# Kernel optimization log

Measured on AMD Instinct MI355X. Metric: run time of the kernel, lower is better.

The kernel has to match this reference:

```python
import jax, jax.numpy as jnp
import numpy as np

B, C, H, W = 4, 64, 128, 128
CQ = C // 8
EPS = 1e-5


def setup_inputs() -> dict:
    key = jax.random.key(0)
    ks = jax.random.split(key, 20)
    r = lambda k, shape, s=0.05: jax.random.normal(k, shape, dtype=jnp.float32) * s
    return {
        "x1": jax.random.normal(ks[0], (B, C, H, W), dtype=jnp.float32),
        "x2": jax.random.normal(ks[1], (B, C, H, W), dtype=jnp.float32),
        # 1x1 convs are plain channel matmuls: weight (out, in), bias (out,)
        "wqA": r(ks[2], (CQ, C)), "bqA": r(ks[3], (CQ,)),
        "wkA": r(ks[4], (CQ, C)), "bkA": r(ks[5], (CQ,)),
        "wvA": r(ks[6], (C, C)),  "bvA": r(ks[7], (C,)),
        "wqB": r(ks[8], (CQ, C)), "bqB": r(ks[9], (CQ,)),
        "wkB": r(ks[10], (CQ, C)), "bkB": r(ks[11], (CQ,)),
        "wvB": r(ks[12], (C, C)),  "bvB": r(ks[13], (C,)),
        "gA": r(ks[14], (1,), 0.1), "gB": r(ks[15], (1,), 0.1),
        "wp": r(ks[16], (C, C)), "bp": r(ks[17], (C,)),
        "bn_g": jnp.ones((C,), dtype=jnp.float32),
        "bn_b": jnp.zeros((C,), dtype=jnp.float32),
    }


def _conv1(x, w, b):
    # 1x1 conv over NCHW == per-pixel channel matmul
    return jnp.einsum('oi,bihw->bohw', w, x) + b[None, :, None, None]


def _axial(q, k, v):
    # criss-cross attention: for each pixel, attend over its row and column,
    # with the column (H) self-position masked to -inf, joint softmax over H+W.
    h = q.shape[2]
    eH = jnp.einsum('bciw,bcjw->biwj', q, k)            # [B,H,W,H] column scores
    eH = jnp.where(jnp.eye(h, dtype=bool)[:, None, :], -jnp.inf, eH)
    eW = jnp.einsum('bchi,bchj->bhij', q, k)            # [B,H,W,W] row scores
    att = jax.nn.softmax(jnp.concatenate([eH, eW], axis=3), axis=3)
    oH = jnp.einsum('bcjw,biwj->bciw', v, att[..., :h])
    oW = jnp.einsum('bchj,bhij->bchi', v, att[..., h:])
    return oH + oW


def _forward(x1, x2, wqA, bqA, wkA, bkA, wvA, bvA, wqB, bqB, wkB, bkB, wvB, bvB,
             gA, gB, wp, bp, bn_g, bn_b):
    # branch A: query from x2, key/value from x1
    out_A = _axial(_conv1(x2, wqA, bqA), _conv1(x1, wkA, bkA), _conv1(x1, wvA, bvA))
    # branch B: query/key/value all from x1
    out_B = _axial(_conv1(x1, wqB, bqB), _conv1(x1, wkB, bkB), _conv1(x1, wvB, bvB))
    diff = jnp.abs(out_A - out_B)
    p = jax.nn.gelu(_conv1(diff, wp, bp), approximate=False)
    # BatchNorm2d in training mode: batch statistics, biased variance
    m = p.mean(axis=(0, 2, 3), keepdims=True)
    v = ((p - m) ** 2).mean(axis=(0, 2, 3), keepdims=True)
    out = (p - m) / jnp.sqrt(v + EPS) * bn_g[None, :, None, None] + bn_b[None, :, None, None]
    return gA[0] * out_A + x1 + out, gB[0] * out_B + x2 + out


def reference(x1, x2, wqA, bqA, wkA, bkA, wvA, bvA, wqB, bqB, wkB, bkB, wvB, bvB,
              gA, gB, wp, bp, bn_g, bn_b):
    return _forward(x1, x2, wqA, bqA, wkA, bkA, wvA, bvA, wqB, bqB, wkB, bkB,
                    wvB, bvB, gA, gB, wp, bp, bn_g, bn_b)
```

## Files before the change

### kernel.cpp

```cpp
#include <hip/hip_runtime.h>


#define NE 4194304ull

typedef __attribute__((ext_vector_type(8))) short short8;
typedef __attribute__((ext_vector_type(4))) float f32x4;

#define HD __device__ __forceinline__

HD float b2f(unsigned short u) { union { unsigned int i; float f; } v; v.i = ((unsigned int)u) << 16; return v.f; }
HD unsigned short f2b(float x) {
  union { float f; unsigned int i; } v; v.f = x;
  unsigned int r = v.i + 0x7FFFu + ((v.i >> 16) & 1u);
  return (unsigned short)(r >> 16);
}

HD float erf_fast(float x) {
  const float ax = fabsf(x);
  const float t = 1.0f / (1.0f + 0.3275911f * ax);
  const float poly = ((((1.061405429f*t - 1.453152027f)*t + 1.421413741f)*t
                       - 0.284496736f)*t + 0.254829592f)*t;
  const float y = 1.0f - poly * __expf(-ax*ax);
  return copysignf(y, x);
}

HD unsigned short ldbf(const void* s0, int i, int f) {
  return f ? f2b(((const float*)s0)[i]) : ((const unsigned short*)s0)[i];
}

__global__ __launch_bounds__(256) void prelude_kernel(
    const void* x1,
    const void* wqA, const void* bqA, const void* wkA, const void* bkA,
    const void* wvA, const void* bvA, const void* wqB, const void* bqB,
    const void* wkB, const void* bkB, const void* wvB, const void* bvB,
    const void* wp, const void* bp, const void* gA, const void* gB,
    const void* bng, const void* bnb,
    int* flag, unsigned short* wout)
{
  __shared__ int s;
  if (threadIdx.x == 0) s = 0;
  __syncthreads();
  const float a = fabsf(b2f(((const unsigned short*)x1)[threadIdx.x]));
  if (a > 1000.0f) atomicOr(&s, 1);
  __syncthreads();
  const int f = s;
  if (blockIdx.x == 0 && threadIdx.x == 0) *flag = f;

  const void* srcs[18] = {wqA,bqA,wkA,bkA,wvA,bvA,wqB,bqB,wkB,bkB,wvB,bvB,wp,bp,gA,gB,bng,bnb};
  const int   ns[18]   = {512,  8,512,  8,4096, 64,512,  8,512,  8,4096, 64,4096,64, 1, 1, 64, 64};
  unsigned short* wqkv = wout + 14696;
  float* wbias = (float*)(wout + 25960);

  const int gstride = gridDim.x * 256;
  for (int idx = blockIdx.x*256 + threadIdx.x; idx < 26136; idx += gstride) {
    if (idx < 14690) {
      int off = idx, k2 = 0;
      while (off >= ns[k2]) { off -= ns[k2]; ++k2; }
      wout[idx] = ldbf(srcs[k2], off, f);
    } else if (idx >= 25960) {
      const int i3 = idx - 25960, mt = i3 >> 4, r = i3 & 15;
      float val = 0.0f;
      if (mt == 0)      { if (r < 8) val = b2f(ldbf(bqA, r, f)); }
      else if (mt == 1) { val = b2f((r < 8) ? ldbf(bkA, r, f) : ldbf(bqB, r - 8, f)); }
      else if (mt == 2) { if (r < 8) val = b2f(ldbf(bkB, r, f)); }
      else if (mt < 7)  { val = b2f(ldbf(bvA, (mt-3)*16 + r, f)); }
      else              { val = b2f(ldbf(bvB, (mt-7)*16 + r, f)); }
      wbias[i3] = val;
    } else if (idx >= 14696) {
      const int i2 = idx - 14696;
      const int mt = i2 >> 10, rem = i2 & 1023, r = rem >> 6, ci = rem & 63;
      unsigned short val = 0;
      if (mt == 0)      { if (r < 8) val = ldbf(wqA, r*64 + ci, f); }
      else if (mt == 1) { val = (r < 8) ? ldbf(wkA, r*64 + ci, f) : ldbf(wqB, (r-8)*64 + ci, f); }
      else if (mt == 2) { if (r < 8) val = ldbf(wkB, r*64 + ci, f); }
      else if (mt < 7)  { val = ldbf(wvA, ((mt-3)*16 + r)*64 + ci, f); }
      else              { val = ldbf(wvB, ((mt-7)*16 + r)*64 + ci, f); }
      wqkv[i2] = val;
    }
  }
}

__global__ __launch_bounds__(256) void qkv_kernel(
    const void* __restrict__ x1v, const void* __restrict__ x2v, const int* __restrict__ flag,
    const unsigned short* __restrict__ wqkv, const float* __restrict__ wbias,
    unsigned short* __restrict__ q, unsigned short* __restrict__ k,
    unsigned short* __restrict__ v)
{
  const int hp = blockIdx.x, b = blockIdx.y;
  const int h0 = hp*2;
  const int tid = threadIdx.x, lane = tid & 63, w4 = tid >> 6;
  const int col = lane & 15, quad = lane >> 4;
  const int f32m = *flag;
  __shared__ __align__(16) char smem[33792];
  unsigned short* Xb = (unsigned short*)smem;
  unsigned short* S0 = (unsigned short*)smem;
  unsigned short* S1 = (unsigned short*)(smem + 8448);
  const size_t gb = (size_t)b*1048576 + (size_t)h0*128;

  short8 Bc[2][8];
  #pragma unroll
  for (int pass = 0; pass < 2; ++pass) {
    const void* xv = pass ? x2v : x1v;
    for (int t = tid; t < 2048; t += 256) {
      const int c = t >> 5, rem = t & 31, hh = rem >> 4, w8 = (rem & 15)*8;
      const int n = hh*128 + w8;
      const size_t a = gb + (size_t)c*16384 + (size_t)hh*128 + w8;
      unsigned short vals[8];
      if (f32m) {
        const float* xf = (const float*)xv;
        const float4 f0 = *(const float4*)(xf + a);
        const float4 f1 = *(const float4*)(xf + a + 4);
        vals[0]=f2b(f0.x); vals[1]=f2b(f0.y); vals[2]=f2b(f0.z); vals[3]=f2b(f0.w);
        vals[4]=f2b(f1.x); vals[5]=f2b(f1.y); vals[6]=f2b(f1.z); vals[7]=f2b(f1.w);
      } else {
        const uint4 u = *(const uint4*)((const unsigned short*)xv + a);
        vals[0]=(unsigned short)(u.x & 0xffff); vals[1]=(unsigned short)(u.x >> 16);
        vals[2]=(unsigned short)(u.y & 0xffff); vals[3]=(unsigned short)(u.y >> 16);
        vals[4]=(unsigned short)(u.z & 0xffff); vals[5]=(unsigned short)(u.z >> 16);
        vals[6]=(unsigned short)(u.w & 0xffff); vals[7]=(unsigned short)(u.w >> 16);
      }
      #pragma unroll
      for (int i = 0; i < 8; ++i) Xb[(n + i)*66 + c] = vals[i];
    }
    __syncthreads();
    const unsigned int* U = (const unsigned int*)Xb;
    #pragma unroll
    for (int nt = 0; nt < 4; ++nt)
      #pragma unroll
      for (int ks = 0; ks < 2; ++ks) {
        const int n = w4*64 + nt*16 + col;
        const int base = n*33 + (ks*32 + quad*8)/2;
        union { unsigned int u32[4]; short8 s; } p;
        #pragma unroll
        for (int jj = 0; jj < 4; ++jj) p.u32[jj] = U[base + jj];
        Bc[pass][nt*2 + ks] = p.s;
      }
    __syncthreads();
  }

  #pragma unroll
  for (int mt = 0; mt < 11; ++mt) {
    f32x4 acc[4];
    #pragma unroll
    for (int nt = 0; nt < 4; ++nt) acc[nt] = (f32x4){0.f, 0.f, 0.f, 0.f};
    #pragma unroll
    for (int ks = 0; ks < 2; ++ks) {
      union { uint4 u; short8 s; } A;
      A.u = *(const uint4*)(wqkv + mt*1024 + col*64 + ks*32 + quad*8);
      #pragma unroll
      for (int nt = 0; nt < 4; ++nt)
        acc[nt] = __builtin_amdgcn_mfma_f32_16x16x32_bf16(
            A.s, (mt == 0) ? Bc[1][nt*2 + ks] : Bc[0][nt*2 + ks], acc[nt], 0, 0, 0);
    }
    float bias[4];
    #pragma unroll
    for (int r = 0; r < 4; ++r) bias[r] = wbias[mt*16 + quad*4 + r];
    unsigned short* S = (mt & 1) ? S1 : S0;
    #pragma unroll
    for (int nt = 0; nt < 4; ++nt)
      #pragma unroll
      for (int r = 0; r < 4; ++r) {
        const int row = quad*4 + r;
        const int nloc = w4*64 + nt*16 + col;
        S[row*264 + nloc] = f2b(acc[nt][r] + bias[r]);
      }
    __syncthreads();
    if (mt < 3) {
      const int nloc = tid;
      const int pixg = h0*128 + nloc;
      union { unsigned short u[8]; uint4 v4; } P;
      #pragma unroll
      for (int r = 0; r < 8; ++r) P.u[r] = S[r*264 + nloc];
      if (mt == 0) {
        *(uint4*)(q + ((size_t)b*16384 + pixg)*8) = P.v4;
      } else if (mt == 1) {
        *(uint4*)(k + ((size_t)b*16384 + pixg)*8) = P.v4;
        #pragma unroll
        for (int r = 0; r < 8; ++r) P.u[r] = S[(8 + r)*264 + nloc];
        *(uint4*)(q + ((size_t)(4 + b)*16384 + pixg)*8) = P.v4;
      } else {
        *(uint4*)(k + ((size_t)(4 + b)*16384 + pixg)*8) = P.v4;
      }
    } else {
      const int vm = (mt >= 7) ? mt - 7 : mt - 3;
      const int z  = (mt >= 7) ? 4 + b : b;
      const int cl = tid >> 4, u = tid & 15;
      const int co = vm*16 + cl;
      const uint4 a0 = *(const uint4*)&S[cl*264 + u*16];
      const uint4 a1 = *(const uint4*)&S[cl*264 + u*16 + 8];
      unsigned short* dst = v + ((size_t)(z*64 + co)*16384 + (size_t)h0*128 + u*16);
      *(uint4*)dst = a0;
      *(uint4*)(dst + 8) = a1;
    }
  }
}

__global__ __launch_bounds__(256) void transpose_v(
    const unsigned short* __restrict__ vStd, unsigned short* __restrict__ vT)
{
  const int tile = blockIdx.x, c = blockIdx.y, z = blockIdx.z;
  const int h0 = (tile & 3) * 32, w0 = (tile >> 2) * 32;
  const size_t base = ((size_t)z*64 + c) * 16384;
  __shared__ unsigned short T[32][33];
  const int tid = threadIdx.x;
  for (int idx = tid; idx < 1024; idx += 256) {
    const int r = idx >> 5, cc = idx & 31;
    T[r][cc] = vStd[base + (size_t)(h0 + r)*128 + (w0 + cc)];
  }
  __syncthreads();
  for (int idx = tid; idx < 1024; idx += 256) {
    const int r = idx >> 5, cc = idx & 31;
    vT[base + (size_t)(w0 + r)*128 + (h0 + cc)] = T[cc][r];
  }
}

__global__ __launch_bounds__(256) void pv_kernel(
    const unsigned short* __restrict__ q, const unsigned short* __restrict__ k,
    const unsigned short* __restrict__ vStd, const unsigned short* __restrict__ vT,
    float* __restrict__ outBrF, float* __restrict__ oColF,
    float* __restrict__ lRow, float* __restrict__ lCol)
{
  const int X = blockIdx.x, b = blockIdx.y;
  const int br = blockIdx.z & 1, dir = blockIdx.z >> 1;
  const int tid = threadIdx.x, lane = tid & 63, w4 = tid >> 6;
  const int col = lane & 15, quad = lane >> 4;
  const int z = br*4 + b;
  const size_t b4h = (size_t)z * 128;
  __shared__ __align__(16) char smemA[34048];
  __shared__ __align__(16) char smemB[16384];
  unsigned short* P = (unsigned short*)smemA;
  float* Dst = (float*)smemA;
  uint4* Ks = (uint4*)smemB;
  uint4* Vl = (uint4*)smemB;

  if (tid < 128) {
    const int j = tid;
    const size_t pix = (b4h + (dir ? X : j))*128 + (dir ? j : X);
    Ks[j] = *(const uint4*)(k + pix*8);
  }
  __syncthreads();

  const uint4 zero4 = {0u, 0u, 0u, 0u};
  short8 Afr[2];
  #pragma unroll
  for (int ib2 = 0; ib2 < 2; ++ib2) {
    uint4 a = zero4;
    if (quad == 0) {
      const int m = (w4*2 + ib2)*16 + col;
      const size_t pix = (b4h + (dir ? X : m))*128 + (dir ? m : X);
      a = *(const uint4*)(q + pix*8);
    }
    union { uint4 u; short8 s; } cv; cv.u = a; Afr[ib2] = cv.s;
  }
  float lsum[2][4];
  #pragma unroll
  for (int ib2 = 0; ib2 < 2; ++ib2)
    #pragma unroll
    for (int r = 0; r < 4; ++r) lsum[ib2][r] = 0.0f;
  #pragma unroll
  for (int nb = 0; nb < 8; ++nb) {
    uint4 bu = (quad == 0) ? Ks[nb*16 + col] : zero4;
    union { uint4 u; short8 s; } bv; bv.u = bu;
    f32x4 sA = __builtin_amdgcn_mfma_f32_16x16x32_bf16(Afr[0], bv.s, (f32x4){0.f,0.f,0.f,0.f}, 0, 0, 0);
    f32x4 sB = __builtin_amdgcn_mfma_f32_16x16x32_bf16(Afr[1], bv.s, (f32x4){0.f,0.f,0.f,0.f}, 0, 0, 0);
    const int j = nb*16 + col;
    #pragma unroll
    for (int ib2 = 0; ib2 < 2; ++ib2) {
      const int mbase = (w4*2 + ib2)*16 + quad*4;
      #pragma unroll
      for (int r = 0; r < 4; ++r) {
        const int m = mbase + r;
        const float sv = ib2 ? sB[r] : sA[r];
        float p = 0.0f;
        if (dir || (j != m)) p = __expf(sv);
        lsum[ib2][r] += p;
        P[m*132 + j] = f2b(p);
      }
    }
  }
  #pragma unroll
  for (int ib2 = 0; ib2 < 2; ++ib2)
    #pragma unroll
    for (int r = 0; r < 4; ++r) {
      float s = lsum[ib2][r];
      s += __shfl_xor(s, 1); s += __shfl_xor(s, 2);
      s += __shfl_xor(s, 4); s += __shfl_xor(s, 8);
      if (col == 0) {
        const int m = (w4*2 + ib2)*16 + quad*4 + r;
        float* lOut = dir ? lRow : lCol;
        lOut[((size_t)z*128 + X)*128 + m] = s;
      }
    }
  __syncthreads();

  short8 af[2][4];
  #pragma unroll
  for (int ib2 = 0; ib2 < 2; ++ib2) {
    const int m = (w4*2 + ib2)*16 + col;
    #pragma unroll
    for (int kb = 0; kb < 4; ++kb) {
      const int j0 = kb*32 + quad*8;
      union { uint2 u[2]; short8 s; } pk;
      pk.u[0] = *(const uint2*)&P[m*132 + j0];
      pk.u[1] = *(const uint2*)&P[m*132 + j0 + 4];
      af[ib2][kb] = pk.s;
    }
  }
  const unsigned short* vsrc = dir ? vStd : vT;
  const size_t vbase = ((size_t)z*64)*16384 + (size_t)X*128;
  for (int t = tid; t < 1024; t += 256) {
    const int vl = t & 63, nb = (t >> 6) & 3, kb = t >> 8;
    const int c = nb*16 + (vl & 15), j0 = kb*32 + ((vl >> 4) << 3);
    Vl[t] = *(const uint4*)(vsrc + vbase + (size_t)c*16384 + j0);
  }
  __syncthreads();

  f32x4 acc[2][4];
  #pragma unroll
  for (int i2 = 0; i2 < 2; ++i2)
    #pragma unroll
    for (int nb = 0; nb < 4; ++nb) acc[i2][nb] = (f32x4){0.f, 0.f, 0.f, 0.f};
  #pragma unroll
  for (int nb = 0; nb < 4; ++nb)
    #pragma unroll
    for (int kb = 0; kb < 4; ++kb) {
      const short8 bfr = *(short8*)&Vl[(kb*4 + nb)*64 + lane];
      acc[0][nb] = __builtin_amdgcn_mfma_f32_16x16x32_bf16(af[0][kb], bfr, acc[0][nb], 0, 0, 0);
      acc[1][nb] = __builtin_amdgcn_mfma_f32_16x16x32_bf16(af[1][kb], bfr, acc[1][nb], 0, 0, 0);
    }
  __syncthreads();

  #pragma unroll
  for (int i2 = 0; i2 < 2; ++i2)
    #pragma unroll
    for (int nb = 0; nb < 4; ++nb)
      #pragma unroll
      for (int r = 0; r < 4; ++r) {
        const int mm = (w4*2 + i2)*16 + ((lane >> 4) << 2) + r;
        const int cc = nb*16 + (lane & 15);
        Dst[cc*133 + mm] = acc[i2][nb][r];
      }
  __syncthreads();
  float* dst = dir ? outBrF : oColF;
  for (int t = tid; t < 8192; t += 256) {
    const int cc = t >> 7, mm = t & 127;
    dst[vbase + (size_t)cc*16384 + mm] = Dst[cc*133 + mm];
  }
}

__global__ __launch_bounds__(256) void combine_kernel(
    const float* __restrict__ oColU, const float* __restrict__ lRow,
    const float* __restrict__ lCol, float* __restrict__ outBr)
{
  const int tile = blockIdx.x, z = blockIdx.y, cg = blockIdx.z;
  const int h0 = (tile & 3) * 32, w0 = (tile >> 2) * 32, c0 = cg*8;
  const int tid = threadIdx.x;
  __shared__ float Tl[32][33];
  __shared__ __align__(16) float inv[32][36];
  __shared__ __align__(16) float T4[4][32][36];
  const size_t lzb = (size_t)z * 16384;
  {
    const int w = tid >> 3, h4 = (tid & 7)*4;
    const float4 vc = *(const float4*)(lCol + lzb + (size_t)(w0 + w)*128 + h0 + h4);
    Tl[w][h4+0] = vc.x; Tl[w][h4+1] = vc.y; Tl[w][h4+2] = vc.z; Tl[w][h4+3] = vc.w;
  }
  __syncthreads();
  {
    const int h = tid >> 3, w4 = (tid & 7)*4;
    const float4 lr = *(const float4*)(lRow + lzb + (size_t)(h0 + h)*128 + w0 + w4);
    float4 iv;
    iv.x = 1.0f / (lr.x + Tl[w4+0][h]);
    iv.y = 1.0f / (lr.y + Tl[w4+1][h]);
    iv.z = 1.0f / (lr.z + Tl[w4+2][h]);
    iv.w = 1.0f / (lr.w + Tl[w4+3][h]);
    *(float4*)&inv[h][w4] = iv;
  }
  __syncthreads();
  #pragma unroll
  for (int half = 0; half < 2; ++half) {
    for (int t = tid; t < 1024; t += 256) {
      const int ch = t >> 8, rem = t & 255, w = rem >> 3, h4 = (rem & 7)*4;
      const int c = c0 + half*4 + ch;
      const float4 vc = *(const float4*)(oColU + ((size_t)(z*64 + c))*16384
                                         + (size_t)(w0 + w)*128 + h0 + h4);
      *(float4*)&T4[ch][w][h4] = vc;
    }
    __syncthreads();
    for (int t = tid; t < 1024; t += 256) {
      const int ch = t >> 8, rem = t & 255, h = rem >> 3, w4 = (rem & 7)*4;
      const int c = c0 + half*4 + ch;
      const size_t off = ((size_t)(z*64 + c))*16384 + (size_t)(h0 + h)*128 + w0 + w4;
      float4 o = *(const float4*)(outBr + off);
      const float4 iv = *(const float4*)&inv[h][w4];
      o.x = (o.x + T4[ch][w4+0][h]) * iv.x;
      o.y = (o.y + T4[ch][w4+1][h]) * iv.y;
      o.z = (o.z + T4[ch][w4+2][h]) * iv.z;
      o.w = (o.w + T4[ch][w4+3][h]) * iv.w;
      *(float4*)(outBr + off) = o;
    }
    __syncthreads();
  }
}

__global__ __launch_bounds__(256) void proj_kernel(
    const float* __restrict__ outA, const float* __restrict__ outB,
    const unsigned short* __restrict__ wp, const unsigned short* __restrict__ bp,
    float* __restrict__ pbuf, float* __restrict__ part)
{
  const int h = blockIdx.x, b = blockIdx.y, wh = blockIdx.z, tid = threadIdx.x;
  const int blk = ((h*4 + b)*2 + wh);
  __shared__ __align__(16) float diffs[64][64];
  for (int idx = tid; idx < 4096; idx += 256) {
    const int c = idx >> 6, w = idx & 63;
    const size_t off = ((size_t)(b*64 + c)*128 + h)*128 + wh*64 + w;
    diffs[c][w] = fabsf(outA[off] - outB[off]);
  }
  __syncthreads();
  const int cog = tid >> 5, wl = tid & 31;
  float acc[8][2];
  #pragma unroll
  for (int c8 = 0; c8 < 8; ++c8) { acc[c8][0] = 0.f; acc[c8][1] = 0.f; }
  for (int cb = 0; cb < 8; ++cb) {
    uint4 wrow[8];
    #pragma unroll
    for (int c8 = 0; c8 < 8; ++c8) wrow[c8] = *(const uint4*)&wp[(cog*8 + c8)*64 + cb*8];
    #pragma unroll
    for (int t = 0; t < 8; ++t) {
      const int ci = cb*8 + t;
      const float d0 = diffs[ci][wl], d1 = diffs[ci][wl + 32];
      #pragma unroll
      for (int c8 = 0; c8 < 8; ++c8) {
        const float wf = b2f(((const unsigned short*)&wrow[c8])[t]);
        acc[c8][0] += wf*d0; acc[c8][1] += wf*d1;
      }
    }
  }
  #pragma unroll
  for (int c8 = 0; c8 < 8; ++c8) {
    const int co = cog*8 + c8;
    const float bias = b2f(bp[co]);
    const size_t pb = ((size_t)(b*64 + co)*128 + h)*128 + wh*64;
    float s1 = 0.f, s2 = 0.f;
    #pragma unroll
    for (int t = 0; t < 2; ++t) {
      const float x = acc[c8][t] + bias;
      const float g = 0.5f * x * (1.0f + erf_fast(x * 0.70710678118f));
      pbuf[pb + wl + t*32] = g;
      s1 += g; s2 += g*g;
    }
    #pragma unroll
    for (int off = 16; off >= 1; off >>= 1) { s1 += __shfl_xor(s1, off); s2 += __shfl_xor(s2, off); }
    if (wl == 0) {
      part[(size_t)co*1024 + blk] = s1;
      part[(size_t)(64 + co)*1024 + blk] = s2;
    }
  }
}

__global__ __launch_bounds__(256) void reduce_kernel(
    const float* __restrict__ part, float* __restrict__ bnAcc)
{
  const int stat = blockIdx.x, tid = threadIdx.x;
  const float4 v = *(const float4*)(part + (size_t)stat*1024 + tid*4);
  float s = v.x + v.y + v.z + v.w;
  #pragma unroll
  for (int off = 32; off >= 1; off >>= 1) s += __shfl_xor(s, off);
  __shared__ float ws4[4];
  if ((tid & 63) == 0) ws4[tid >> 6] = s;
  __syncthreads();
  if (tid == 0) bnAcc[stat] = ws4[0] + ws4[1] + ws4[2] + ws4[3];
}

__global__ __launch_bounds__(256) void final_kernel(
    const float* __restrict__ pbuf, const float* __restrict__ outA, const float* __restrict__ outB,
    const void* __restrict__ x1v, const void* __restrict__ x2v, const int* __restrict__ flag,
    const unsigned short* __restrict__ gA, const unsigned short* __restrict__ gB,
    const unsigned short* __restrict__ bng, const unsigned short* __restrict__ bnb,
    const float* __restrict__ bnAcc, void* __restrict__ outv)
{
  const int f32m = *flag;
  const int idx = (blockIdx.x * 256 + threadIdx.x) * 4;
  const int c = (idx >> 14) & 63;
  const float invN = 1.0f / 65536.0f;
  const float s1 = bnAcc[c], s2 = bnAcc[64 + c];
  const float mean = s1 * invN;
  const float var = s2 * invN - mean*mean;
  const float scale = rsqrtf(var + 1e-5f) * b2f(bng[c]);
  const float beta = b2f(bnb[c]);
  const float ga = b2f(gA[0]), gb = b2f(gB[0]);
  const float4 p4 = *(const float4*)(pbuf + idx);
  const float4 a4 = *(const float4*)(outA + idx);
  const float4 b4 = *(const float4*)(outB + idx);
  float p[4] = {p4.x, p4.y, p4.z, p4.w};
  float a[4] = {a4.x, a4.y, a4.z, a4.w};
  float bb[4] = {b4.x, b4.y, b4.z, b4.w};
  float xa[4], xb[4];
  if (f32m) {
    const float4 t1 = *(const float4*)((const float*)x1v + idx);
    const float4 t2 = *(const float4*)((const float*)x2v + idx);
    xa[0]=t1.x; xa[1]=t1.y; xa[2]=t1.z; xa[3]=t1.w;
    xb[0]=t2.x; xb[1]=t2.y; xb[2]=t2.z; xb[3]=t2.w;
  } else {
    const uint2 x1u = *(const uint2*)((const unsigned short*)x1v + idx);
    const uint2 x2u = *(const uint2*)((const unsigned short*)x2v + idx);
    xa[0] = b2f((unsigned short)(x1u.x & 0xffff)); xa[1] = b2f((unsigned short)(x1u.x >> 16));
    xa[2] = b2f((unsigned short)(x1u.y & 0xffff)); xa[3] = b2f((unsigned short)(x1u.y >> 16));
    xb[0] = b2f((unsigned short)(x2u.x & 0xffff)); xb[1] = b2f((unsigned short)(x2u.x >> 16));
    xb[2] = b2f((unsigned short)(x2u.y & 0xffff)); xb[3] = b2f((unsigned short)(x2u.y >> 16));
  }
  float o1f[4], o2f[4];
  #pragma unroll
  for (int t = 0; t < 4; ++t) {
    const float nv = (p[t] - mean)*scale + beta;
    o1f[t] = ga*a[t] + xa[t] + nv;
    o2f[t] = gb*bb[t] + xb[t] + nv;
  }
  if (f32m) {
    float* of = (float*)outv;
    *(float4*)(of + idx)      = (float4){o1f[0], o1f[1], o1f[2], o1f[3]};
    *(float4*)(of + NE + idx) = (float4){o2f[0], o2f[1], o2f[2], o2f[3]};
  } else {
    unsigned short* oh = (unsigned short*)outv;
    uint2 u1, u2;
    u1.x = (unsigned int)f2b(o1f[0]) | ((unsigned int)f2b(o1f[1]) << 16);
    u1.y = (unsigned int)f2b(o1f[2]) | ((unsigned int)f2b(o1f[3]) << 16);
    u2.x = (unsigned int)f2b(o2f[0]) | ((unsigned int)f2b(o2f[1]) << 16);
    u2.y = (unsigned int)f2b(o2f[2]) | ((unsigned int)f2b(o2f[3]) << 16);
    *(uint2*)(oh + idx) = u1;
    *(uint2*)(oh + NE + idx) = u2;
  }
}

extern "C" void kernel_launch(void* const* d_in, const int* in_sizes, int n_in,
                              void* d_out, int out_size, void* d_ws, size_t ws_size,
                              hipStream_t stream)
{
  const void* x1  = d_in[0];
  const void* x2  = d_in[1];

  char* ws = (char*)d_ws;
  const size_t MB = 1048576ull;
  unsigned short* q     = (unsigned short*)(ws);
  unsigned short* kk    = (unsigned short*)(ws + 2*MB);
  float* lRow           = (float*)(ws + 4*MB);
  float* lCol           = (float*)(ws + 4*MB + 512*1024);
  unsigned short* vStd  = (unsigned short*)(ws + 6*MB);
  unsigned short* vT    = (unsigned short*)(ws + 22*MB);
  float* outBr          = (float*)(ws + 38*MB);
  float* oColF          = (float*)(ws + 70*MB);
  float* pbuf           = (float*)(ws + 70*MB);
  float* part           = (float*)(ws + 86*MB);
  float* bnAcc          = (float*)(ws + 102*MB);
  int*   flag           = (int*)(ws + 102*MB + 512);
  unsigned short* wC    = (unsigned short*)(ws + 102*MB + 1024);

  prelude_kernel<<<64, 256, 0, stream>>>(
      x1, d_in[2], d_in[3], d_in[4], d_in[5], d_in[6], d_in[7], d_in[8], d_in[9],
      d_in[10], d_in[11], d_in[12], d_in[13], d_in[16], d_in[17], d_in[14], d_in[15],
      d_in[18], d_in[19], flag, wC);
  qkv_kernel<<<dim3(64, 4), 256, 0, stream>>>(
      x1, x2, flag, wC + 14696, (const float*)(wC + 25960), q, kk, vStd);
  transpose_v<<<dim3(16, 64, 8), 256, 0, stream>>>(vStd, vT);
  pv_kernel<<<dim3(128, 4, 4), 256, 0, stream>>>(q, kk, vStd, vT, outBr, oColF, lRow, lCol);
  combine_kernel<<<dim3(16, 8, 8), 256, 0, stream>>>(oColF, lRow, lCol, outBr);
  proj_kernel<<<dim3(128, 4, 2), 256, 0, stream>>>(outBr, outBr + NE, wC + 10400, wC + 14496, pbuf, part);
  reduce_kernel<<<128, 256, 0, stream>>>(part, bnAcc);
  final_kernel<<<4096, 256, 0, stream>>>(pbuf, outBr, outBr + NE, x1, x2, flag,
                                         wC + 14560, wC + 14561, wC + 14562, wC + 14626,
                                         bnAcc, d_out);
}
```

Before: 232.2 us.

## Store attention branch outputs in bf16 and move projection onto MFMA

```diff
diff --git a/kernel.cpp b/kernel.cpp
--- a/kernel.cpp
+++ b/kernel.cpp
@@ -217,7 +217,7 @@
 __global__ __launch_bounds__(256) void pv_kernel(
     const unsigned short* __restrict__ q, const unsigned short* __restrict__ k,
     const unsigned short* __restrict__ vStd, const unsigned short* __restrict__ vT,
-    float* __restrict__ outBrF, float* __restrict__ oColF,
+    unsigned short* __restrict__ outBrH, unsigned short* __restrict__ oColH,
     float* __restrict__ lRow, float* __restrict__ lCol)
 {
   const int X = blockIdx.x, b = blockIdx.y;
@@ -341,16 +341,20 @@
         Dst[cc*133 + mm] = acc[i2][nb][r];
       }
   __syncthreads();
-  float* dst = dir ? outBrF : oColF;
-  for (int t = tid; t < 8192; t += 256) {
-    const int cc = t >> 7, mm = t & 127;
-    dst[vbase + (size_t)cc*16384 + mm] = Dst[cc*133 + mm];
+  unsigned short* dsth = dir ? outBrH : oColH;
+  for (int t = tid; t < 2048; t += 256) {
+    const int cc = t >> 5, mm4 = (t & 31) * 4;
+    const float* sp = &Dst[cc*133 + mm4];
+    uint2 u;
+    u.x = (unsigned int)f2b(sp[0]) | ((unsigned int)f2b(sp[1]) << 16);
+    u.y = (unsigned int)f2b(sp[2]) | ((unsigned int)f2b(sp[3]) << 16);
+    *(uint2*)(dsth + vbase + (size_t)cc*16384 + mm4) = u;
   }
 }
 
 __global__ __launch_bounds__(256) void combine_kernel(
-    const float* __restrict__ oColU, const float* __restrict__ lRow,
-    const float* __restrict__ lCol, float* __restrict__ outBr)
+    const unsigned short* __restrict__ oColU, const float* __restrict__ lRow,
+    const float* __restrict__ lCol, unsigned short* __restrict__ outBr)
 {
   const int tile = blockIdx.x, z = blockIdx.y, cg = blockIdx.z;
   const int h0 = (tile & 3) * 32, w0 = (tile >> 2) * 32, c0 = cg*8;
@@ -381,79 +385,121 @@
     for (int t = tid; t < 1024; t += 256) {
       const int ch = t >> 8, rem = t & 255, w = rem >> 3, h4 = (rem & 7)*4;
       const int c = c0 + half*4 + ch;
-      const float4 vc = *(const float4*)(oColU + ((size_t)(z*64 + c))*16384
-                                         + (size_t)(w0 + w)*128 + h0 + h4);
-      *(float4*)&T4[ch][w][h4] = vc;
+      const uint2 vc = *(const uint2*)(oColU + ((size_t)(z*64 + c))*16384
+                                       + (size_t)(w0 + w)*128 + h0 + h4);
+      float4 f;
+      f.x = b2f((unsigned short)(vc.x & 0xffff)); f.y = b2f((unsigned short)(vc.x >> 16));
+      f.z = b2f((unsigned short)(vc.y & 0xffff)); f.w = b2f((unsigned short)(vc.y >> 16));
+      *(float4*)&T4[ch][w][h4] = f;
     }
     __syncthreads();
     for (int t = tid; t < 1024; t += 256) {
       const int ch = t >> 8, rem = t & 255, h = rem >> 3, w4 = (rem & 7)*4;
       const int c = c0 + half*4 + ch;
       const size_t off = ((size_t)(z*64 + c))*16384 + (size_t)(h0 + h)*128 + w0 + w4;
-      float4 o = *(const float4*)(outBr + off);
+      const uint2 ov = *(const uint2*)(outBr + off);
       const float4 iv = *(const float4*)&inv[h][w4];
-      o.x = (o.x + T4[ch][w4+0][h]) * iv.x;
-      o.y = (o.y + T4[ch][w4+1][h]) * iv.y;
-      o.z = (o.z + T4[ch][w4+2][h]) * iv.z;
-      o.w = (o.w + T4[ch][w4+3][h]) * iv.w;
-      *(float4*)(outBr + off) = o;
+      float o0 = b2f((unsigned short)(ov.x & 0xffff));
+      float o1 = b2f((unsigned short)(ov.x >> 16));
+      float o2 = b2f((unsigned short)(ov.y & 0xffff));
+      float o3 = b2f((unsigned short)(ov.y >> 16));
+      o0 = (o0 + T4[ch][w4+0][h]) * iv.x;
+      o1 = (o1 + T4[ch][w4+1][h]) * iv.y;
+      o2 = (o2 + T4[ch][w4+2][h]) * iv.z;
+      o3 = (o3 + T4[ch][w4+3][h]) * iv.w;
+      uint2 u;
+      u.x = (unsigned int)f2b(o0) | ((unsigned int)f2b(o1) << 16);
+      u.y = (unsigned int)f2b(o2) | ((unsigned int)f2b(o3) << 16);
+      *(uint2*)(outBr + off) = u;
     }
     __syncthreads();
   }
 }
 
 __global__ __launch_bounds__(256) void proj_kernel(
-    const float* __restrict__ outA, const float* __restrict__ outB,
+    const unsigned short* __restrict__ outA, const unsigned short* __restrict__ outB,
     const unsigned short* __restrict__ wp, const unsigned short* __restrict__ bp,
     float* __restrict__ pbuf, float* __restrict__ part)
 {
-  const int h = blockIdx.x, b = blockIdx.y, wh = blockIdx.z, tid = threadIdx.x;
-  const int blk = ((h*4 + b)*2 + wh);
-  __shared__ __align__(16) float diffs[64][64];
-  for (int idx = tid; idx < 4096; idx += 256) {
-    const int c = idx >> 6, w = idx & 63;
-    const size_t off = ((size_t)(b*64 + c)*128 + h)*128 + wh*64 + w;
-    diffs[c][w] = fabsf(outA[off] - outB[off]);
-  }
-  __syncthreads();
-  const int cog = tid >> 5, wl = tid & 31;
-  float acc[8][2];
-  #pragma unroll
-  for (int c8 = 0; c8 < 8; ++c8) { acc[c8][0] = 0.f; acc[c8][1] = 0.f; }
-  for (int cb = 0; cb < 8; ++cb) {
-    uint4 wrow[8];
-    #pragma unroll
-    for (int c8 = 0; c8 < 8; ++c8) wrow[c8] = *(const uint4*)&wp[(cog*8 + c8)*64 + cb*8];
-    #pragma unroll
-    for (int t = 0; t < 8; ++t) {
-      const int ci = cb*8 + t;
-      const float d0 = diffs[ci][wl], d1 = diffs[ci][wl + 32];
-      #pragma unroll
-      for (int c8 = 0; c8 < 8; ++c8) {
-        const float wf = b2f(((const unsigned short*)&wrow[c8])[t]);
-        acc[c8][0] += wf*d0; acc[c8][1] += wf*d1;
-      }
-    }
-  }
-  #pragma unroll
-  for (int c8 = 0; c8 < 8; ++c8) {
-    const int co = cog*8 + c8;
-    const float bias = b2f(bp[co]);
-    const size_t pb = ((size_t)(b*64 + co)*128 + h)*128 + wh*64;
-    float s1 = 0.f, s2 = 0.f;
-    #pragma unroll
-    for (int t = 0; t < 2; ++t) {
-      const float x = acc[c8][t] + bias;
+  const int hp = blockIdx.x, b = blockIdx.y;
+  const int tid = threadIdx.x, lane = tid & 63, w4 = tid >> 6;
+  const int col = lane & 15, quad = lane >> 4;
+  __shared__ __align__(16) char smem[17408];
+  unsigned short* Xb = (unsigned short*)smem;
+  float* S = (float*)smem;
+
+  const size_t gb = (size_t)b*1048576 + (size_t)hp*64;
+  for (int t = tid; t < 512; t += 256) {
+    const int c = t >> 3, rem = t & 7;
+    const size_t a = gb + (size_t)c*16384 + rem*8;
+    const uint4 ua = *(const uint4*)(outA + a);
+    const uint4 ub = *(const uint4*)(outB + a);
+    const unsigned short* pa = (const unsigned short*)&ua;
+    const unsigned short* pb = (const unsigned short*)&ub;
+    const int n = rem*8;
+    #pragma unroll
+    for (int i = 0; i < 8; ++i)
+      Xb[(n + i)*66 + c] = f2b(fabsf(b2f(pa[i]) - b2f(pb[i])));
+  }
+  __syncthreads();
+
+  short8 Bc[8];
+  const unsigned int* U = (const unsigned int*)Xb;
+  #pragma unroll
+  for (int nt = 0; nt < 4; ++nt)
+    #pragma unroll
+    for (int ks = 0; ks < 2; ++ks) {
+      const int n = nt*16 + col;
+      const int base = n*33 + (ks*32 + quad*8)/2;
+      union { unsigned int u32[4]; short8 s; } p;
+      #pragma unroll
+      for (int jj = 0; jj < 4; ++jj) p.u32[jj] = U[base + jj];
+      Bc[nt*2 + ks] = p.s;
+    }
+  __syncthreads();
+
+  f32x4 acc[4];
+  #pragma unroll
+  for (int nt = 0; nt < 4; ++nt) acc[nt] = (f32x4){0.f, 0.f, 0.f, 0.f};
+  #pragma unroll
+  for (int ks = 0; ks < 2; ++ks) {
+    union { uint4 u; short8 s; } A;
+    A.u = *(const uint4*)(wp + (w4*16 + col)*64 + ks*32 + quad*8);
+    #pragma unroll
+    for (int nt = 0; nt < 4; ++nt)
+      acc[nt] = __builtin_amdgcn_mfma_f32_16x16x32_bf16(A.s, Bc[nt*2 + ks], acc[nt], 0, 0, 0);
+  }
+
+  float sg1[4] = {0.f, 0.f, 0.f, 0.f}, sg2[4] = {0.f, 0.f, 0.f, 0.f};
+  #pragma unroll
+  for (int nt = 0; nt < 4; ++nt)
+    #pragma unroll
+    for (int r = 0; r < 4; ++r) {
+      const float x = acc[nt][r] + b2f(bp[w4*16 + quad*4 + r]);
       const float g = 0.5f * x * (1.0f + erf_fast(x * 0.70710678118f));
-      pbuf[pb + wl + t*32] = g;
-      s1 += g; s2 += g*g;
-    }
-    #pragma unroll
-    for (int off = 16; off >= 1; off >>= 1) { s1 += __shfl_xor(s1, off); s2 += __shfl_xor(s2, off); }
-    if (wl == 0) {
-      part[(size_t)co*1024 + blk] = s1;
-      part[(size_t)(64 + co)*1024 + blk] = s2;
-    }
+      S[(w4*16 + quad*4 + r)*68 + nt*16 + col] = g;
+      sg1[r] += g; sg2[r] += g*g;
+    }
+  const int slot = hp*4 + b;
+  #pragma unroll
+  for (int r = 0; r < 4; ++r) {
+    float s1 = sg1[r], s2 = sg2[r];
+    s1 += __shfl_xor(s1, 1); s1 += __shfl_xor(s1, 2);
+    s1 += __shfl_xor(s1, 4); s1 += __shfl_xor(s1, 8);
+    s2 += __shfl_xor(s2, 1); s2 += __shfl_xor(s2, 2);
+    s2 += __shfl_xor(s2, 4); s2 += __shfl_xor(s2, 8);
+    if (col == 0) {
+      const int co = w4*16 + quad*4 + r;
+      part[(size_t)co*1024 + slot] = s1;
+      part[(size_t)(64 + co)*1024 + slot] = s2;
+    }
+  }
+  __syncthreads();
+
+  for (int t = tid; t < 1024; t += 256) {
+    const int row = t >> 4, px4 = (t & 15)*4;
+    const float4 v4 = *(const float4*)&S[row*68 + px4];
+    *(float4*)(pbuf + (size_t)(b*64 + row)*16384 + hp*64 + px4) = v4;
   }
 }
 
@@ -472,7 +518,8 @@
 }
 
 __global__ __launch_bounds__(256) void final_kernel(
-    const float* __restrict__ pbuf, const float* __restrict__ outA, const float* __restrict__ outB,
+    const float* __restrict__ pbuf,
+    const unsigned short* __restrict__ outAH, const unsigned short* __restrict__ outBH,
     const void* __restrict__ x1v, const void* __restrict__ x2v, const int* __restrict__ flag,
     const unsigned short* __restrict__ gA, const unsigned short* __restrict__ gB,
     const unsigned short* __restrict__ bng, const unsigned short* __restrict__ bnb,
@@ -489,11 +536,13 @@
   const float beta = b2f(bnb[c]);
   const float ga = b2f(gA[0]), gb = b2f(gB[0]);
   const float4 p4 = *(const float4*)(pbuf + idx);
-  const float4 a4 = *(const float4*)(outA + idx);
-  const float4 b4 = *(const float4*)(outB + idx);
+  const uint2 uA = *(const uint2*)(outAH + idx);
+  const uint2 uB = *(const uint2*)(outBH + idx);
   float p[4] = {p4.x, p4.y, p4.z, p4.w};
-  float a[4] = {a4.x, a4.y, a4.z, a4.w};
-  float bb[4] = {b4.x, b4.y, b4.z, b4.w};
+  float a[4] = { b2f((unsigned short)(uA.x & 0xffff)), b2f((unsigned short)(uA.x >> 16)),
+                 b2f((unsigned short)(uA.y & 0xffff)), b2f((unsigned short)(uA.y >> 16)) };
+  float bb[4] = { b2f((unsigned short)(uB.x & 0xffff)), b2f((unsigned short)(uB.x >> 16)),
+                  b2f((unsigned short)(uB.y & 0xffff)), b2f((unsigned short)(uB.y >> 16)) };
   float xa[4], xb[4];
   if (f32m) {
     const float4 t1 = *(const float4*)((const float*)x1v + idx);
@@ -546,8 +595,8 @@
   float* lCol           = (float*)(ws + 4*MB + 512*1024);
   unsigned short* vStd  = (unsigned short*)(ws + 6*MB);
   unsigned short* vT    = (unsigned short*)(ws + 22*MB);
-  float* outBr          = (float*)(ws + 38*MB);
-  float* oColF          = (float*)(ws + 70*MB);
+  unsigned short* outBrH= (unsigned short*)(ws + 38*MB);
+  unsigned short* oColH = (unsigned short*)(ws + 54*MB);
   float* pbuf           = (float*)(ws + 70*MB);
   float* part           = (float*)(ws + 86*MB);
   float* bnAcc          = (float*)(ws + 102*MB);
@@ -561,11 +610,11 @@
   qkv_kernel<<<dim3(64, 4), 256, 0, stream>>>(
       x1, x2, flag, wC + 14696, (const float*)(wC + 25960), q, kk, vStd);
   transpose_v<<<dim3(16, 64, 8), 256, 0, stream>>>(vStd, vT);
-  pv_kernel<<<dim3(128, 4, 4), 256, 0, stream>>>(q, kk, vStd, vT, outBr, oColF, lRow, lCol);
-  combine_kernel<<<dim3(16, 8, 8), 256, 0, stream>>>(oColF, lRow, lCol, outBr);
-  proj_kernel<<<dim3(128, 4, 2), 256, 0, stream>>>(outBr, outBr + NE, wC + 10400, wC + 14496, pbuf, part);
+  pv_kernel<<<dim3(128, 4, 4), 256, 0, stream>>>(q, kk, vStd, vT, outBrH, oColH, lRow, lCol);
+  combine_kernel<<<dim3(16, 8, 8), 256, 0, stream>>>(oColH, lRow, lCol, outBrH);
+  proj_kernel<<<dim3(256, 4), 256, 0, stream>>>(outBrH, outBrH + NE, wC + 10400, wC + 14496, pbuf, part);
   reduce_kernel<<<128, 256, 0, stream>>>(part, bnAcc);
-  final_kernel<<<4096, 256, 0, stream>>>(pbuf, outBr, outBr + NE, x1, x2, flag,
+  final_kernel<<<4096, 256, 0, stream>>>(pbuf, outBrH, outBrH + NE, x1, x2, flag,
                                          wC + 14560, wC + 14561, wC + 14562, wC + 14626,
                                          bnAcc, d_out);
 }
```

New measurement: 216.2 us. -6.9%, faster.
